# Kernel tuning notes

Hardware: AMD Instinct MI355X
Metric: run time of the kernel (lower is better)

Reference implementation:

```python
import jax, jax.numpy as jnp
import numpy as np

B, L, D = 2, 2048, 1024
N_HEADS, N_KV_HEADS = 16, 4
HEAD_DIM = D // N_HEADS
WINDOW = 1024
ROPE_BASE = 10000.0


def setup_inputs() -> dict:
    key = jax.random.key(0)
    ks = jax.random.split(key, 5)
    s = 0.02
    return {
        "x": jax.random.normal(ks[0], (B, L, D), jnp.float32),
        "Wq": jax.random.normal(ks[1], (D, N_HEADS * HEAD_DIM), jnp.float32) * s,
        "Wk": jax.random.normal(ks[2], (D, N_KV_HEADS * HEAD_DIM), jnp.float32) * s,
        "Wv": jax.random.normal(ks[3], (D, N_KV_HEADS * HEAD_DIM), jnp.float32) * s,
        "Wo": jax.random.normal(ks[4], (N_HEADS * HEAD_DIM, D), jnp.float32) * s,
    }


def _rope_cos_sin(seq_len, head_dim, dtype):
    inv_freq = 1.0 / (ROPE_BASE ** (jnp.arange(0, head_dim, 2, dtype=jnp.float32) / head_dim))
    angles = jnp.arange(seq_len, dtype=jnp.float32)[:, None] * inv_freq[None, :]  # [L, d/2]
    emb = jnp.concatenate([angles, angles], axis=-1)  # [L, d]
    return jnp.cos(emb).astype(dtype), jnp.sin(emb).astype(dtype)


def _rotate_half(t):
    t1, t2 = jnp.split(t, 2, axis=-1)
    return jnp.concatenate([-t2, t1], axis=-1)


def reference(x, Wq, Wk, Wv, Wo):
    b, l, d = x.shape
    q = (x @ Wq).reshape(b, l, N_HEADS, HEAD_DIM).transpose(0, 2, 1, 3)      # [B,H,L,d]
    k = (x @ Wk).reshape(b, l, N_KV_HEADS, HEAD_DIM).transpose(0, 2, 1, 3)   # [B,Kv,L,d]
    v = (x @ Wv).reshape(b, l, N_KV_HEADS, HEAD_DIM).transpose(0, 2, 1, 3)

    cos, sin = _rope_cos_sin(l, HEAD_DIM, x.dtype)  # [L,d]
    q = q * cos[None, None] + _rotate_half(q) * sin[None, None]
    k = k * cos[None, None] + _rotate_half(k) * sin[None, None]

    # GQA: expand kv heads to query heads
    group = N_HEADS // N_KV_HEADS
    k = jnp.repeat(k, group, axis=1)  # [B,H,L,d]
    v = jnp.repeat(v, group, axis=1)

    scale = 1.0 / np.sqrt(HEAD_DIM)
    scores = jnp.einsum("bhqd,bhkd->bhqk", q, k) * scale  # [B,H,L,L]

    # sliding-window causal mask: attend to j with j <= i and i - j < WINDOW
    i = jnp.arange(l)[:, None]
    j = jnp.arange(l)[None, :]
    allowed = (j <= i) & (i - j < WINDOW)
    scores = jnp.where(allowed[None, None], scores, jnp.finfo(scores.dtype).min)

    attn = jax.nn.softmax(scores, axis=-1)
    out = jnp.einsum("bhqk,bhkd->bhqd", attn, v)           # [B,H,L,d]
    out = out.transpose(0, 2, 1, 3).reshape(b, l, N_HEADS * HEAD_DIM)
    return out @ Wo  # [B,L,D]; dropout p=0 is identity
```

## Files before the change

### kernel.cpp

```cpp
#include <hip/hip_runtime.h>

typedef unsigned short u16;
typedef unsigned int u32;
typedef short short8 __attribute__((ext_vector_type(8)));
typedef float f32x4 __attribute__((ext_vector_type(4)));

#define N_B 2
#define N_L 2048
#define N_D 1024
#define N_H 16
#define N_KVH 4
#define HDIM 64
#define WINDOW 1024

#define QSCALE (0.125f * 1.44269504088896f)

__device__ __forceinline__ u16 f2bf(float f) {
  unsigned u = __builtin_bit_cast(unsigned, f);
  u = u + 0x7fffu + ((u >> 16) & 1u);
  return (u16)(u >> 16);
}

__device__ __forceinline__ u32 pk2bf(float lo, float hi) {
  u32 a = __builtin_bit_cast(u32, lo) + 0x8000u;
  u32 b = __builtin_bit_cast(u32, hi) + 0x8000u;
  return __builtin_amdgcn_perm(b, a, 0x07060302u);
}

__device__ __forceinline__ void gl2lds16(const u16* g, u16* l) {
  __builtin_amdgcn_global_load_lds((const __attribute__((address_space(1))) void*)g,
                                   (__attribute__((address_space(3))) void*)l, 16, 0, 0);
}


__global__ __launch_bounds__(256) void prep_kernel(
    const float* __restrict__ x, const float* __restrict__ Wq, const float* __restrict__ Wk,
    const float* __restrict__ Wv, const float* __restrict__ Wo,
    u16* __restrict__ xb, u16* __restrict__ wqkvT, u16* __restrict__ woT,
    float* __restrict__ rc, float* __restrict__ rs) {
  __shared__ float tbuf[32][33];
  int bid = blockIdx.x, tid = threadIdx.x;
  if (bid < 1024) {
    size_t base = ((size_t)bid * 256 + tid) * 16;
    u32 o[8];
#pragma unroll
    for (int j = 0; j < 4; j++) {
      float4 f = *(const float4*)&x[base + j * 4];
      o[2 * j] = pk2bf(f.x, f.y);
      o[2 * j + 1] = pk2bf(f.z, f.w);
    }
    *(uint4*)&xb[base] = *(uint4*)&o[0];
    *(uint4*)&xb[base + 8] = *(uint4*)&o[4];
  } else if (bid < 3584) {
    const float* src;
    u16* dst;
    int gx, t, shift;
    if (bid < 2048) { src = Wq; dst = wqkvT; gx = 32; shift = 5; t = bid - 1024; }
    else if (bid < 2304) { src = Wk; dst = wqkvT + 1024 * 1024; gx = 8; shift = 3; t = bid - 2048; }
    else if (bid < 2560) { src = Wv; dst = wqkvT + 1280 * 1024; gx = 8; shift = 3; t = bid - 2304; }
    else { src = Wo; dst = woT; gx = 32; shift = 5; t = bid - 2560; }
    int srcN = gx * 32;
    int n0 = (t & (gx - 1)) * 32, k0 = (t >> shift) * 32;
    int lx = tid & 31, ly = tid >> 5;
#pragma unroll
    for (int q = 0; q < 4; q++)
      tbuf[ly + 8 * q][lx] = src[(k0 + ly + 8 * q) * srcN + n0 + lx];
    __syncthreads();
#pragma unroll
    for (int q = 0; q < 4; q++)
      dst[(n0 + ly + 8 * q) * 1024 + k0 + lx] = f2bf(tbuf[lx][ly + 8 * q]);
  } else {
    int idx = (bid - 3584) * 256 + tid;
    int i = idx >> 5, j = idx & 31;
    float inv = powf(10000.0f, -(float)j * (1.0f / 32.0f));
    float ang = (float)i * inv;
    rc[idx] = cosf(ang);
    rs[idx] = sinf(ang);
  }
}


template <int MODE>
__global__ __launch_bounds__(256, 2) void gemm_kernel(
    const u16* __restrict__ A, const u16* __restrict__ Bt,
    u16* __restrict__ qo, u16* __restrict__ ko, u16* __restrict__ vo,
    float* __restrict__ fo, const float* __restrict__ rc, const float* __restrict__ rs) {
  __shared__ u16 smem[65536 / 2];
  int tid = threadIdx.x;
  int w = tid >> 6, lane = tid & 63, quad = lane >> 4, r = lane & 15;
  int rx = r & 7;
  int wm = w >> 1, wn = w & 1;
  int m0 = blockIdx.y * 128, n0 = blockIdx.x * 128;

  f32x4 acc[4][4];
#pragma unroll
  for (int a_ = 0; a_ < 4; a_++)
#pragma unroll
    for (int b_ = 0; b_ < 4; b_++) acc[a_][b_] = {0.f, 0.f, 0.f, 0.f};

  auto stage = [&](int kt, int buf) {
    u16* a_s = smem + buf * 8192;
    u16* b_s = smem + 16384 + buf * 8192;
#pragma unroll
    for (int it = 0; it < 4; ++it) {
      int cc = it * 256 + tid;
      int row = cc >> 3, p = cc & 7, c = p ^ (row & 7);
      gl2lds16(&A[(size_t)(m0 + row) * 1024 + kt * 64 + c * 8], &a_s[cc * 8]);
    }
#pragma unroll
    for (int it = 0; it < 4; ++it) {
      int cc = it * 256 + tid;
      int row = cc >> 3, p = cc & 7, c = p ^ (row & 7);
      gl2lds16(&Bt[(size_t)(n0 + row) * 1024 + kt * 64 + c * 8], &b_s[cc * 8]);
    }
  };

  stage(0, 0);
  for (int kt = 0; kt < 16; ++kt) {
    int buf = kt & 1;
    __syncthreads();
    if (kt + 1 < 16) stage(kt + 1, buf ^ 1);
    u16* a_s = smem + buf * 8192;
    u16* b_s = smem + 16384 + buf * 8192;
#pragma unroll
    for (int ks = 0; ks < 2; ks++) {
      int pc = (ks * 4 + quad) ^ rx;
      short8 af[4], bfr[4];
#pragma unroll
      for (int tm = 0; tm < 4; tm++)
        af[tm] = *(const short8*)&a_s[(wm * 64 + tm * 16 + r) * 64 + pc * 8];
#pragma unroll
      for (int tn = 0; tn < 4; tn++)
        bfr[tn] = *(const short8*)&b_s[(wn * 64 + tn * 16 + r) * 64 + pc * 8];
#pragma unroll
      for (int tm = 0; tm < 4; tm++)
#pragma unroll
        for (int tn = 0; tn < 4; tn++)
          acc[tm][tn] = __builtin_amdgcn_mfma_f32_16x16x32_bf16(af[tm], bfr[tn], acc[tm][tn], 0, 0, 0);
    }
    __syncthreads();
  }

  int nbase = n0 + wn * 64;
  if constexpr (MODE == 0) {
    if (nbase < 1024) {
      int h = nbase >> 6;
#pragma unroll
      for (int tm = 0; tm < 4; tm++) {
#pragma unroll
        for (int reg = 0; reg < 4; reg++) {
          int m = m0 + wm * 64 + tm * 16 + quad * 4 + reg;
          int b = m >> 11, i = m & 2047;
          size_t base = ((size_t)(b * N_H + h) * N_L + i) * HDIM;
#pragma unroll
          for (int tn = 0; tn < 2; tn++) {
            int dlo = tn * 16 + r;
            float c = rc[i * 32 + dlo], s = rs[i * 32 + dlo];
            float vlo = acc[tm][tn][reg], vhi = acc[tm][tn + 2][reg];
            qo[base + dlo] = f2bf((vlo * c - vhi * s) * QSCALE);
            qo[base + dlo + 32] = f2bf((vhi * c + vlo * s) * QSCALE);
          }
        }
      }
    } else if (nbase < 1280) {
      int h = (nbase - 1024) >> 6;
#pragma unroll
      for (int tm = 0; tm < 4; tm++) {
#pragma unroll
        for (int reg = 0; reg < 4; reg++) {
          int m = m0 + wm * 64 + tm * 16 + quad * 4 + reg;
          int b = m >> 11, i = m & 2047;
          size_t base = ((size_t)(b * N_KVH + h) * N_L + i) * HDIM;
#pragma unroll
          for (int tn = 0; tn < 2; tn++) {
            int dlo = tn * 16 + r;
            float c = rc[i * 32 + dlo], s = rs[i * 32 + dlo];
            float vlo = acc[tm][tn][reg], vhi = acc[tm][tn + 2][reg];
            ko[base + dlo] = f2bf(vlo * c - vhi * s);
            ko[base + dlo + 32] = f2bf(vhi * c + vlo * s);
          }
        }
      }
    } else {
      __syncthreads();
      int hkv = (nbase - 1280) >> 6;
      int bb = (m0 + wm * 64) >> 11;
      int tbase = (m0 + wm * 64) & 2047;
      u16* myvs = smem + w * 4608;
#pragma unroll
      for (int tm = 0; tm < 4; tm++) {
#pragma unroll
        for (int tn = 0; tn < 4; tn++) {
          uint2 pk;
          pk.x = pk2bf(acc[tm][tn][0], acc[tm][tn][1]);
          pk.y = pk2bf(acc[tm][tn][2], acc[tm][tn][3]);
          *(uint2*)&myvs[(tn * 16 + r) * 72 + tm * 16 + quad * 4] = pk;
        }
      }
      __asm__ volatile("s_waitcnt lgkmcnt(0)" ::: "memory");
      u16* vtb = vo + (size_t)((bb * N_KVH + hkv) * 64) * 2048;
#pragma unroll
      for (int q2 = 0; q2 < 8; ++q2) {
        int flat = q2 * 64 + lane;
        int row = flat >> 3, part = flat & 7;
        uint4 val = *(uint4*)&myvs[row * 72 + part * 8];
        *(uint4*)&vtb[row * 2048 + tbase + part * 8] = val;
      }
    }
  } else {
#pragma unroll
    for (int tm = 0; tm < 4; tm++) {
#pragma unroll
      for (int reg = 0; reg < 4; reg++) {
        int m = m0 + wm * 64 + tm * 16 + quad * 4 + reg;
#pragma unroll
        for (int tn = 0; tn < 4; tn++)
          fo[(size_t)m * 1024 + nbase + tn * 16 + r] = acc[tm][tn][reg];
      }
    }
  }
}


__global__ __launch_bounds__(256) void attn_kernel(
    const u16* __restrict__ Q, const u16* __restrict__ K,
    const u16* __restrict__ Vt, u16* __restrict__ O) {
  __shared__ u16 k_s[2][64 * 64];
  __shared__ u16 v_s[2][64 * 64];
  __shared__ u16 pt[4][16 * 64];
  int tid = threadIdx.x, w = tid >> 6, lane = tid & 63, quad = lane >> 4, r = lane & 15;
  int qb = 31 - blockIdx.x;
  int h = blockIdx.y, b = blockIdx.z;
  int i0 = qb * 64;
  int hk = h >> 2;
  int qw0 = i0 + w * 16;
  int iq = qw0 + r;

  const u16* qptr = Q + (size_t)((b * N_H + h) * N_L + iq) * HDIM;
  short8 qf[2];
  qf[0] = *(const short8*)&qptr[quad * 8];
  qf[1] = *(const short8*)&qptr[32 + quad * 8];

  const u16* kbase = K + (size_t)(b * N_KVH + hk) * N_L * HDIM;
  const u16* vtbase = Vt + (size_t)(b * N_KVH + hk) * HDIM * N_L;

  auto stage = [&](int jt, int buf) {
#pragma unroll
    for (int it = 0; it < 2; ++it) {
      int cc = it * 256 + tid;
      int row = cc >> 3, p = cc & 7, c = p ^ (row & 7);
      gl2lds16(&kbase[(size_t)(jt * 64 + row) * 64 + c * 8], &k_s[buf][cc * 8]);
    }
#pragma unroll
    for (int it = 0; it < 2; ++it) {
      int cc = it * 256 + tid;
      int row = cc >> 3, p = cc & 7, c = p ^ (row & 7);
      gl2lds16(&vtbase[(size_t)row * 2048 + jt * 64 + c * 8], &v_s[buf][cc * 8]);
    }
  };

  float l_lane = 0.f;
  f32x4 o_acc[4];
#pragma unroll
  for (int tm = 0; tm < 4; tm++) o_acc[tm] = {0.f, 0.f, 0.f, 0.f};

  int jt0 = (i0 >= WINDOW) ? ((i0 - (WINDOW - 1)) >> 6) : 0;
  int nt = qb - jt0 + 1;
  u16* mypt = pt[w];
  int rx = r & 7;

  stage(jt0, 0);

  for (int t = 0; t < nt; ++t) {
    int jt = jt0 + t, j0 = jt << 6, buf = t & 1;
    __syncthreads();
    if (t + 1 < nt) stage(jt + 1, buf ^ 1);

    f32x4 s_acc[4];
#pragma unroll
    for (int tm = 0; tm < 4; tm++) s_acc[tm] = {0.f, 0.f, 0.f, 0.f};
#pragma unroll
    for (int ks = 0; ks < 2; ks++) {
      int pc = (ks * 4 + quad) ^ rx;
#pragma unroll
      for (int tm = 0; tm < 4; tm++) {
        short8 kf = *(const short8*)&k_s[buf][(tm * 16 + r) * 64 + pc * 8];
        s_acc[tm] = __builtin_amdgcn_mfma_f32_16x16x32_bf16(kf, qf[ks], s_acc[tm], 0, 0, 0);
      }
    }

    bool interior = (j0 + 63 <= qw0) && (qw0 + 15 - j0 < WINDOW);
    if (!interior) {
#pragma unroll
      for (int tm = 0; tm < 4; tm++) {
#pragma unroll
        for (int reg = 0; reg < 4; reg++) {
          int j = j0 + tm * 16 + quad * 4 + reg;
          bool ok = (j <= iq) && (iq - j < WINDOW);
          if (!ok) s_acc[tm][reg] = -1e30f;
        }
      }
    }

    float p[4][4];
#pragma unroll
    for (int tm = 0; tm < 4; tm++)
#pragma unroll
      for (int reg = 0; reg < 4; reg++) {
        float e = __builtin_amdgcn_exp2f(s_acc[tm][reg]);
        p[tm][reg] = e;
        l_lane += e;
      }

#pragma unroll
    for (int tm = 0; tm < 4; tm++) {
      uint2 pk;
      pk.x = pk2bf(p[tm][0], p[tm][1]);
      pk.y = pk2bf(p[tm][2], p[tm][3]);
      int c = tm * 2 + (quad >> 1), half = quad & 1;
      int pp = c ^ rx;
      *(uint2*)&mypt[r * 64 + pp * 8 + half * 4] = pk;
    }
    __asm__ volatile("s_waitcnt lgkmcnt(0)" ::: "memory");

#pragma unroll
    for (int ks = 0; ks < 2; ks++) {
      int pc = (ks * 4 + quad) ^ rx;
      short8 bp = *(const short8*)&mypt[r * 64 + pc * 8];
#pragma unroll
      for (int tm = 0; tm < 4; tm++) {
        short8 av = *(const short8*)&v_s[buf][(tm * 16 + r) * 64 + pc * 8];
        o_acc[tm] = __builtin_amdgcn_mfma_f32_16x16x32_bf16(av, bp, o_acc[tm], 0, 0, 0);
      }
    }
  }

  l_lane += __shfl_xor(l_lane, 16);
  l_lane += __shfl_xor(l_lane, 32);
  float inv = 1.0f / l_lane;
  size_t obase = (size_t)(b * N_L + iq) * 1024 + h * 64;
#pragma unroll
  for (int tm = 0; tm < 4; tm++) {
    uint2 pk;
    pk.x = pk2bf(o_acc[tm][0] * inv, o_acc[tm][1] * inv);
    pk.y = pk2bf(o_acc[tm][2] * inv, o_acc[tm][3] * inv);
    *(uint2*)&O[obase + tm * 16 + quad * 4] = pk;
  }
}


extern "C" void kernel_launch(void* const* d_in, const int* in_sizes, int n_in,
                              void* d_out, int out_size, void* d_ws, size_t ws_size,
                              hipStream_t stream) {
  const float* x = (const float*)d_in[0];
  const float* Wq = (const float*)d_in[1];
  const float* Wk = (const float*)d_in[2];
  const float* Wv = (const float*)d_in[3];
  const float* Wo = (const float*)d_in[4];
  float* out = (float*)d_out;
  char* ws = (char*)d_ws;

  u16* xb    = (u16*)(ws);
  u16* wqkvT = (u16*)(ws + 0x800000);
  u16* woT   = (u16*)(ws + 0xB00000);
  u16* Qb    = (u16*)(ws + 0xD00000);
  u16* Kb    = (u16*)(ws + 0x1500000);
  u16* Vtb   = (u16*)(ws + 0x1700000);
  u16* Ob    = (u16*)(ws + 0x1900000);
  float* rc  = (float*)(ws + 0x2100000);
  float* rs  = (float*)(ws + 0x2140000);

  prep_kernel<<<3840, 256, 0, stream>>>(x, Wq, Wk, Wv, Wo, xb, wqkvT, woT, rc, rs);
  gemm_kernel<0><<<dim3(12, 32), 256, 0, stream>>>(xb, wqkvT, Qb, Kb, Vtb, nullptr, rc, rs);
  attn_kernel<<<dim3(32, 16, 2), 256, 0, stream>>>(Qb, Kb, Vtb, Ob);
  gemm_kernel<1><<<dim3(8, 32), 256, 0, stream>>>(Ob, woT, nullptr, nullptr, nullptr, out, nullptr, nullptr);
}
```

Before: 150.9 us.

## Split attention keys across waves, split-K output GEMM with atomics, drop sync

The attention kernel now gives each wave a 16-key slice of every key tile for all 64 queries, instead of 16 queries across all keys. Probabilities stay in registers and feed a 16x16x16 MFMA directly, which removes the P round-trip through LDS. Per-wave partial outputs and row sums are then reduced through shared memory at the end. The output projection becomes a split-K GEMM over two z-slices that accumulates into an output zeroed by memset, using float atomics; this doubles block count at the cost of atomic traffic and an extra memset. The trailing __syncthreads in the GEMM k-loop is also removed, relying on the next iteration's barrier for buffer reuse.

```diff
diff --git a/kernel.cpp b/kernel.cpp
--- a/kernel.cpp
+++ b/kernel.cpp
@@ -3,6 +3,7 @@
 typedef unsigned short u16;
 typedef unsigned int u32;
 typedef short short8 __attribute__((ext_vector_type(8)));
+typedef short s16x4 __attribute__((ext_vector_type(4)));
 typedef float f32x4 __attribute__((ext_vector_type(4)));
 
 #define N_B 2
@@ -30,6 +31,14 @@
 __device__ __forceinline__ void gl2lds16(const u16* g, u16* l) {
   __builtin_amdgcn_global_load_lds((const __attribute__((address_space(1))) void*)g,
                                    (__attribute__((address_space(3))) void*)l, 16, 0, 0);
+}
+
+__device__ __forceinline__ f32x4 mfma16(s16x4 a, s16x4 b, f32x4 c) {
+#if __has_builtin(__builtin_amdgcn_mfma_f32_16x16x16_bf16)
+  return __builtin_amdgcn_mfma_f32_16x16x16_bf16(a, b, c, 0, 0, 0);
+#else
+  return __builtin_amdgcn_mfma_f32_16x16x16bf16_1k(a, b, c, 0, 0, 0);
+#endif
 }
 
 
@@ -91,6 +100,8 @@
   int rx = r & 7;
   int wm = w >> 1, wn = w & 1;
   int m0 = blockIdx.y * 128, n0 = blockIdx.x * 128;
+  constexpr int NKT = (MODE == 2) ? 8 : 16;
+  int koff = (MODE == 2) ? blockIdx.z * NKT : 0;
 
   f32x4 acc[4][4];
 #pragma unroll
@@ -105,21 +116,21 @@
     for (int it = 0; it < 4; ++it) {
       int cc = it * 256 + tid;
       int row = cc >> 3, p = cc & 7, c = p ^ (row & 7);
-      gl2lds16(&A[(size_t)(m0 + row) * 1024 + kt * 64 + c * 8], &a_s[cc * 8]);
+      gl2lds16(&A[(size_t)(m0 + row) * 1024 + (koff + kt) * 64 + c * 8], &a_s[cc * 8]);
     }
 #pragma unroll
     for (int it = 0; it < 4; ++it) {
       int cc = it * 256 + tid;
       int row = cc >> 3, p = cc & 7, c = p ^ (row & 7);
-      gl2lds16(&Bt[(size_t)(n0 + row) * 1024 + kt * 64 + c * 8], &b_s[cc * 8]);
+      gl2lds16(&Bt[(size_t)(n0 + row) * 1024 + (koff + kt) * 64 + c * 8], &b_s[cc * 8]);
     }
   };
 
   stage(0, 0);
-  for (int kt = 0; kt < 16; ++kt) {
+  for (int kt = 0; kt < NKT; ++kt) {
     int buf = kt & 1;
     __syncthreads();
-    if (kt + 1 < 16) stage(kt + 1, buf ^ 1);
+    if (kt + 1 < NKT) stage(kt + 1, buf ^ 1);
     u16* a_s = smem + buf * 8192;
     u16* b_s = smem + 16384 + buf * 8192;
 #pragma unroll
@@ -138,7 +149,6 @@
         for (int tn = 0; tn < 4; tn++)
           acc[tm][tn] = __builtin_amdgcn_mfma_f32_16x16x32_bf16(af[tm], bfr[tn], acc[tm][tn], 0, 0, 0);
     }
-    __syncthreads();
   }
 
   int nbase = n0 + wn * 64;
@@ -215,7 +225,7 @@
         int m = m0 + wm * 64 + tm * 16 + quad * 4 + reg;
 #pragma unroll
         for (int tn = 0; tn < 4; tn++)
-          fo[(size_t)m * 1024 + nbase + tn * 16 + r] = acc[tm][tn][reg];
+          unsafeAtomicAdd(&fo[(size_t)m * 1024 + nbase + tn * 16 + r], acc[tm][tn][reg]);
       }
     }
   }
@@ -225,49 +235,52 @@
 __global__ __launch_bounds__(256) void attn_kernel(
     const u16* __restrict__ Q, const u16* __restrict__ K,
     const u16* __restrict__ Vt, u16* __restrict__ O) {
-  __shared__ u16 k_s[2][64 * 64];
-  __shared__ u16 v_s[2][64 * 64];
-  __shared__ u16 pt[4][16 * 64];
+  __shared__ __align__(16) u16 smem[16384];
+  __shared__ float l_s[256];
   int tid = threadIdx.x, w = tid >> 6, lane = tid & 63, quad = lane >> 4, r = lane & 15;
   int qb = 31 - blockIdx.x;
   int h = blockIdx.y, b = blockIdx.z;
   int i0 = qb * 64;
   int hk = h >> 2;
-  int qw0 = i0 + w * 16;
-  int iq = qw0 + r;
-
-  const u16* qptr = Q + (size_t)((b * N_H + h) * N_L + iq) * HDIM;
-  short8 qf[2];
-  qf[0] = *(const short8*)&qptr[quad * 8];
-  qf[1] = *(const short8*)&qptr[32 + quad * 8];
+  int rx = r & 7;
+
+  const u16* qbase = Q + (size_t)((b * N_H + h) * N_L + i0) * HDIM;
+  short8 qf[4][2];
+#pragma unroll
+  for (int tn = 0; tn < 4; tn++)
+#pragma unroll
+    for (int ks = 0; ks < 2; ks++)
+      qf[tn][ks] = *(const short8*)&qbase[(size_t)(tn * 16 + r) * 64 + ks * 32 + quad * 8];
 
   const u16* kbase = K + (size_t)(b * N_KVH + hk) * N_L * HDIM;
   const u16* vtbase = Vt + (size_t)(b * N_KVH + hk) * HDIM * N_L;
 
   auto stage = [&](int jt, int buf) {
+    u16* ksb = smem + buf * 4096;
+    u16* vsb = smem + 8192 + buf * 4096;
 #pragma unroll
     for (int it = 0; it < 2; ++it) {
       int cc = it * 256 + tid;
       int row = cc >> 3, p = cc & 7, c = p ^ (row & 7);
-      gl2lds16(&kbase[(size_t)(jt * 64 + row) * 64 + c * 8], &k_s[buf][cc * 8]);
+      gl2lds16(&kbase[(size_t)(jt * 64 + row) * 64 + c * 8], &ksb[cc * 8]);
     }
 #pragma unroll
     for (int it = 0; it < 2; ++it) {
       int cc = it * 256 + tid;
       int row = cc >> 3, p = cc & 7, c = p ^ (row & 7);
-      gl2lds16(&vtbase[(size_t)row * 2048 + jt * 64 + c * 8], &v_s[buf][cc * 8]);
+      gl2lds16(&vtbase[(size_t)row * 2048 + jt * 64 + c * 8], &vsb[cc * 8]);
     }
   };
 
-  float l_lane = 0.f;
-  f32x4 o_acc[4];
-#pragma unroll
-  for (int tm = 0; tm < 4; tm++) o_acc[tm] = {0.f, 0.f, 0.f, 0.f};
+  float l_acc[4] = {0.f, 0.f, 0.f, 0.f};
+  f32x4 o_acc[4][4];
+#pragma unroll
+  for (int tm = 0; tm < 4; tm++)
+#pragma unroll
+    for (int tn = 0; tn < 4; tn++) o_acc[tm][tn] = {0.f, 0.f, 0.f, 0.f};
 
   int jt0 = (i0 >= WINDOW) ? ((i0 - (WINDOW - 1)) >> 6) : 0;
   int nt = qb - jt0 + 1;
-  u16* mypt = pt[w];
-  int rx = r & 7;
 
   stage(jt0, 0);
 
@@ -275,76 +288,118 @@
     int jt = jt0 + t, j0 = jt << 6, buf = t & 1;
     __syncthreads();
     if (t + 1 < nt) stage(jt + 1, buf ^ 1);
+    u16* ksb = smem + buf * 4096;
+    u16* vsb = smem + 8192 + buf * 4096;
 
     f32x4 s_acc[4];
 #pragma unroll
-    for (int tm = 0; tm < 4; tm++) s_acc[tm] = {0.f, 0.f, 0.f, 0.f};
+    for (int tn = 0; tn < 4; tn++) s_acc[tn] = {0.f, 0.f, 0.f, 0.f};
 #pragma unroll
     for (int ks = 0; ks < 2; ks++) {
       int pc = (ks * 4 + quad) ^ rx;
-#pragma unroll
-      for (int tm = 0; tm < 4; tm++) {
-        short8 kf = *(const short8*)&k_s[buf][(tm * 16 + r) * 64 + pc * 8];
-        s_acc[tm] = __builtin_amdgcn_mfma_f32_16x16x32_bf16(kf, qf[ks], s_acc[tm], 0, 0, 0);
-      }
-    }
-
-    bool interior = (j0 + 63 <= qw0) && (qw0 + 15 - j0 < WINDOW);
+      short8 kf = *(const short8*)&ksb[(w * 16 + r) * 64 + pc * 8];
+#pragma unroll
+      for (int tn = 0; tn < 4; tn++)
+        s_acc[tn] = __builtin_amdgcn_mfma_f32_16x16x32_bf16(kf, qf[tn][ks], s_acc[tn], 0, 0, 0);
+    }
+
+    int jw = j0 + w * 16;
+    bool interior = (jw + 15 <= i0) && ((i0 + 63 - jw) < WINDOW);
     if (!interior) {
 #pragma unroll
-      for (int tm = 0; tm < 4; tm++) {
+      for (int tn = 0; tn < 4; tn++) {
 #pragma unroll
         for (int reg = 0; reg < 4; reg++) {
-          int j = j0 + tm * 16 + quad * 4 + reg;
-          bool ok = (j <= iq) && (iq - j < WINDOW);
-          if (!ok) s_acc[tm][reg] = -1e30f;
+          int j = jw + quad * 4 + reg;
+          int i = i0 + tn * 16 + r;
+          bool ok = (j <= i) && (i - j < WINDOW);
+          if (!ok) s_acc[tn][reg] = -1e30f;
         }
       }
     }
 
-    float p[4][4];
+    s16x4 pf[4];
+#pragma unroll
+    for (int tn = 0; tn < 4; tn++) {
+      float e0 = __builtin_amdgcn_exp2f(s_acc[tn][0]);
+      float e1 = __builtin_amdgcn_exp2f(s_acc[tn][1]);
+      float e2 = __builtin_amdgcn_exp2f(s_acc[tn][2]);
+      float e3 = __builtin_amdgcn_exp2f(s_acc[tn][3]);
+      l_acc[tn] += (e0 + e1) + (e2 + e3);
+      union { u32 u[2]; s16x4 s; } pu;
+      pu.u[0] = pk2bf(e0, e1);
+      pu.u[1] = pk2bf(e2, e3);
+      pf[tn] = pu.s;
+    }
+
+    int vcol = w * 16 + quad * 4;
+    int vchunk = vcol >> 3, voff = vcol & 7;
+#pragma unroll
+    for (int tm = 0; tm < 4; tm++) {
+      int pp = vchunk ^ rx;
+      s16x4 va = *(const s16x4*)&vsb[(tm * 16 + r) * 64 + pp * 8 + voff];
+#pragma unroll
+      for (int tn = 0; tn < 4; tn++)
+        o_acc[tm][tn] = mfma16(va, pf[tn], o_acc[tm][tn]);
+    }
+  }
+
+#pragma unroll
+  for (int tn = 0; tn < 4; tn++) {
+    l_acc[tn] += __shfl_xor(l_acc[tn], 16);
+    l_acc[tn] += __shfl_xor(l_acc[tn], 32);
+  }
+  if (quad == 0) {
+#pragma unroll
+    for (int tn = 0; tn < 4; tn++) l_s[w * 64 + tn * 16 + r] = l_acc[tn];
+  }
+  __syncthreads();
+  float* red = (float*)smem;
+  if (w & 1) {
+    int slot = w >> 1;
 #pragma unroll
     for (int tm = 0; tm < 4; tm++)
 #pragma unroll
-      for (int reg = 0; reg < 4; reg++) {
-        float e = __builtin_amdgcn_exp2f(s_acc[tm][reg]);
-        p[tm][reg] = e;
-        l_lane += e;
-      }
-
+      for (int tn = 0; tn < 4; tn++)
+        *(f32x4*)&red[slot * 4096 + tm * 1024 + (tn * 16 + r) * 16 + quad * 4] = o_acc[tm][tn];
+  }
+  __syncthreads();
+  if (!(w & 1)) {
+    int slot = w >> 1;
+#pragma unroll
+    for (int tm = 0; tm < 4; tm++)
+#pragma unroll
+      for (int tn = 0; tn < 4; tn++)
+        o_acc[tm][tn] += *(const f32x4*)&red[slot * 4096 + tm * 1024 + (tn * 16 + r) * 16 + quad * 4];
+  }
+  __syncthreads();
+  if (w == 2) {
+#pragma unroll
+    for (int tm = 0; tm < 4; tm++)
+#pragma unroll
+      for (int tn = 0; tn < 4; tn++)
+        *(f32x4*)&red[tm * 1024 + (tn * 16 + r) * 16 + quad * 4] = o_acc[tm][tn];
+  }
+  __syncthreads();
+  if (w == 0) {
+    float inv[4];
+#pragma unroll
+    for (int tn = 0; tn < 4; tn++) {
+      int q = tn * 16 + r;
+      inv[tn] = 1.0f / (((l_s[q] + l_s[64 + q]) + (l_s[128 + q] + l_s[192 + q])));
+    }
 #pragma unroll
     for (int tm = 0; tm < 4; tm++) {
-      uint2 pk;
-      pk.x = pk2bf(p[tm][0], p[tm][1]);
-      pk.y = pk2bf(p[tm][2], p[tm][3]);
-      int c = tm * 2 + (quad >> 1), half = quad & 1;
-      int pp = c ^ rx;
-      *(uint2*)&mypt[r * 64 + pp * 8 + half * 4] = pk;
-    }
-    __asm__ volatile("s_waitcnt lgkmcnt(0)" ::: "memory");
-
-#pragma unroll
-    for (int ks = 0; ks < 2; ks++) {
-      int pc = (ks * 4 + quad) ^ rx;
-      short8 bp = *(const short8*)&mypt[r * 64 + pc * 8];
-#pragma unroll
-      for (int tm = 0; tm < 4; tm++) {
-        short8 av = *(const short8*)&v_s[buf][(tm * 16 + r) * 64 + pc * 8];
-        o_acc[tm] = __builtin_amdgcn_mfma_f32_16x16x32_bf16(av, bp, o_acc[tm], 0, 0, 0);
-      }
-    }
-  }
-
-  l_lane += __shfl_xor(l_lane, 16);
-  l_lane += __shfl_xor(l_lane, 32);
-  float inv = 1.0f / l_lane;
-  size_t obase = (size_t)(b * N_L + iq) * 1024 + h * 64;
-#pragma unroll
-  for (int tm = 0; tm < 4; tm++) {
-    uint2 pk;
-    pk.x = pk2bf(o_acc[tm][0] * inv, o_acc[tm][1] * inv);
-    pk.y = pk2bf(o_acc[tm][2] * inv, o_acc[tm][3] * inv);
-    *(uint2*)&O[obase + tm * 16 + quad * 4] = pk;
+#pragma unroll
+      for (int tn = 0; tn < 4; tn++) {
+        f32x4 o = o_acc[tm][tn];
+        o += *(const f32x4*)&red[tm * 1024 + (tn * 16 + r) * 16 + quad * 4];
+        uint2 pk;
+        pk.x = pk2bf(o[0] * inv[tn], o[1] * inv[tn]);
+        pk.y = pk2bf(o[2] * inv[tn], o[3] * inv[tn]);
+        *(uint2*)&O[(size_t)(b * N_L + i0 + tn * 16 + r) * 1024 + h * 64 + tm * 16 + quad * 4] = pk;
+      }
+    }
   }
 }
 
@@ -373,5 +428,6 @@
   prep_kernel<<<3840, 256, 0, stream>>>(x, Wq, Wk, Wv, Wo, xb, wqkvT, woT, rc, rs);
   gemm_kernel<0><<<dim3(12, 32), 256, 0, stream>>>(xb, wqkvT, Qb, Kb, Vtb, nullptr, rc, rs);
   attn_kernel<<<dim3(32, 16, 2), 256, 0, stream>>>(Qb, Kb, Vtb, Ob);
-  gemm_kernel<1><<<dim3(8, 32), 256, 0, stream>>>(Ob, woT, nullptr, nullptr, nullptr, out, nullptr, nullptr);
-}
+  (void)hipMemsetAsync(out, 0, (size_t)4096 * 1024 * 4, stream);
+  gemm_kernel<2><<<dim3(8, 32, 2), 256, 0, stream>>>(Ob, woT, nullptr, nullptr, nullptr, out, nullptr, nullptr);
+}
```

Result: slower. 182.3 us (+20.8%).
